# Kernel tuning notes

Hardware: AMD Instinct MI355X
Metric: run time of the kernel (lower is better)

## Reference

```python
import jax, jax.numpy as jnp
import numpy as np

HEADS = 24
HEAD_DIM = 128
DIM = HEADS * HEAD_DIM  # 3072
EPS = 1e-6


def setup_inputs() -> dict:
    key = jax.random.key(0)
    ks = jax.random.split(key, 10)
    B, S_IMG, S_TXT = 1, 2048, 256
    hidden_states = jax.random.normal(ks[0], (B, S_IMG, DIM), jnp.float32)
    encoder_hidden_states = jax.random.normal(ks[1], (B, S_TXT, DIM), jnp.float32)
    # RoPE tables for image tokens, interleaved pair layout [S_IMG, HEAD_DIM]
    inv = 1.0 / (10000.0 ** (np.arange(0, HEAD_DIM, 2, dtype=np.float32) / HEAD_DIM))
    ang = np.arange(S_IMG, dtype=np.float32)[:, None] * inv[None, :]  # [S, Dh/2]
    ang = np.repeat(ang, 2, axis=-1)  # [S, Dh], pairs (2i, 2i+1) share angle
    rope_cos = jnp.asarray(np.cos(ang), jnp.float32)
    rope_sin = jnp.asarray(np.sin(ang), jnp.float32)
    s = 0.02
    wq = jax.random.normal(ks[2], (DIM, DIM), jnp.float32) * s
    wk = jax.random.normal(ks[3], (DIM, DIM), jnp.float32) * s
    wv = jax.random.normal(ks[4], (DIM, DIM), jnp.float32) * s
    wo = jax.random.normal(ks[5], (DIM, DIM), jnp.float32) * s
    bq = jax.random.normal(ks[6], (DIM,), jnp.float32) * s
    bk = jax.random.normal(ks[7], (DIM,), jnp.float32) * s
    bv = jax.random.normal(ks[8], (DIM,), jnp.float32) * s
    bo = jax.random.normal(ks[9], (DIM,), jnp.float32) * s
    norm_q_w = jnp.ones((HEAD_DIM,), jnp.float32)
    norm_k_w = jnp.ones((HEAD_DIM,), jnp.float32)
    return dict(hidden_states=hidden_states, encoder_hidden_states=encoder_hidden_states,
                rope_cos=rope_cos, rope_sin=rope_sin,
                wq=wq, bq=bq, wk=wk, bk=bk, wv=wv, bv=bv,
                norm_q_w=norm_q_w, norm_k_w=norm_k_w, wo=wo, bo=bo)


def _rmsnorm(x, w):
    var = jnp.mean(jnp.square(x), axis=-1, keepdims=True)
    return x * jax.lax.rsqrt(var + EPS) * w


def _rope(x, cos, sin):
    # x [B,H,S,Dh]; diffusers apply_rotary_emb with use_real_unbind_dim=-1:
    # pairs are interleaved (x[2i], x[2i+1]) -> rotated = stack(-imag, real)
    xr = x[..., 0::2]
    xi = x[..., 1::2]
    x_rot = jnp.stack([-xi, xr], axis=-1).reshape(x.shape)
    return x * cos + x_rot * sin


def reference(hidden_states, encoder_hidden_states, rope_cos, rope_sin,
              wq, bq, wk, bk, wv, bv, norm_q_w, norm_k_w, wo, bo):
    B, s_img, D = hidden_states.shape
    s_txt = encoder_hidden_states.shape[1]
    S = s_img + s_txt
    x = jnp.concatenate([hidden_states, encoder_hidden_states], axis=1)  # [B,S,D]

    def proj(w, b):
        return (x @ w + b).reshape(B, S, HEADS, HEAD_DIM).transpose(0, 2, 1, 3)  # [B,H,S,Dh]

    q = _rmsnorm(proj(wq, bq), norm_q_w)
    k = _rmsnorm(proj(wk, bk), norm_k_w)
    v = proj(wv, bv)
    # RoPE on image tokens only
    q = jnp.concatenate([_rope(q[:, :, :s_img], rope_cos, rope_sin), q[:, :, s_img:]], axis=2)
    k = jnp.concatenate([_rope(k[:, :, :s_img], rope_cos, rope_sin), k[:, :, s_img:]], axis=2)
    scale = 1.0 / jnp.sqrt(jnp.float32(HEAD_DIM))
    scores = jnp.einsum('bhqd,bhkd->bhqk', q, k) * scale
    attn = jax.nn.softmax(scores, axis=-1)
    out = jnp.einsum('bhqk,bhkd->bhqd', attn, v)
    out = out.transpose(0, 2, 1, 3).reshape(B, S, D)
    img = out[:, :s_img] @ wo + bo  # to_out[0]; to_out[1] is Dropout(p=0) -> identity
    txt = out[:, s_img:]            # to_add_out is None in this branch
    return img, txt
```

## Files before the change

### kernel.cpp

```cpp
#include <hip/hip_runtime.h>
#include <cstdint>

typedef __bf16 bf16_t;
typedef bf16_t bf16x8 __attribute__((ext_vector_type(8)));
typedef bf16_t bf16x4 __attribute__((ext_vector_type(4)));
typedef float  floatx4 __attribute__((ext_vector_type(4)));

#define S_ALL 2304
#define SIMG  2048
#define NH    24
#define HD    128
#define DIM   3072
#define NQKV  9216

#define SHIFT2 17.312340490667562f
#define QSCALE 0.12751744f

typedef __attribute__((address_space(1))) void* gp1_t;
typedef __attribute__((address_space(3))) void* lp3_t;

__device__ __forceinline__ void async16(const void* g, void* l) {
    __builtin_amdgcn_global_load_lds((gp1_t)(g), (lp3_t)(l), 16, 0, 0);
}
__device__ __forceinline__ floatx4 mfma_bf16(bf16x8 a, bf16x8 b, floatx4 c) {
    return __builtin_amdgcn_mfma_f32_16x16x32_bf16(a, b, c, 0, 0, 0);
}

__global__ __launch_bounds__(256) void k_convert_x(const float* __restrict__ hid,
                                                   const float* __restrict__ enc,
                                                   bf16_t* __restrict__ xb) {
    long i = ((long)blockIdx.x * 256 + threadIdx.x) * 4;
    const long HN = (long)SIMG * DIM;
    float4 f = (i < HN) ? *(const float4*)(hid + i) : *(const float4*)(enc + (i - HN));
    bf16x4 o;
    o[0] = (bf16_t)f.x; o[1] = (bf16_t)f.y; o[2] = (bf16_t)f.z; o[3] = (bf16_t)f.w;
    *(bf16x4*)(xb + i) = o;
}

__global__ __launch_bounds__(256) void k_wT4(const float* __restrict__ wq, const float* __restrict__ wk,
                                             const float* __restrict__ wv, const float* __restrict__ wo,
                                             bf16_t* __restrict__ wTq, bf16_t* __restrict__ woT) {
    __shared__ __align__(16) bf16_t T[64][72];
    int z = blockIdx.z;
    const float* W = (z == 0) ? wq : (z == 1) ? wk : (z == 2) ? wv : wo;
    bf16_t* Wt = (z < 3) ? (wTq + (long)z * DIM * DIM) : woT;
    int r0 = blockIdx.x * 64, c0 = blockIdx.y * 64;
    int tid = threadIdx.x;
    int lr = tid >> 2, lc = (tid & 3) * 16;
    const float* src = W + (long)(r0 + lr) * DIM + c0 + lc;
#pragma unroll
    for (int i = 0; i < 16; i += 4) {
        float4 f = *(const float4*)(src + i);
        T[lr][lc + i + 0] = (bf16_t)f.x;
        T[lr][lc + i + 1] = (bf16_t)f.y;
        T[lr][lc + i + 2] = (bf16_t)f.z;
        T[lr][lc + i + 3] = (bf16_t)f.w;
    }
    __syncthreads();
    bf16x8 a, b;
#pragma unroll
    for (int i = 0; i < 8; i++) a[i] = T[lc + i][lr];
#pragma unroll
    for (int i = 0; i < 8; i++) b[i] = T[lc + 8 + i][lr];
    bf16_t* dst = Wt + (long)(c0 + lr) * DIM + r0 + lc;
    *(bf16x8*)dst = a;
    *(bf16x8*)(dst + 8) = b;
}

__global__ __launch_bounds__(256) void k_gemm_qkv(const bf16_t* __restrict__ A,
                                                  const bf16_t* __restrict__ Bt,
                                                  const float* __restrict__ bq_,
                                                  const float* __restrict__ bk_,
                                                  const float* __restrict__ bv_,
                                                  const float* __restrict__ rope_cos,
                                                  const float* __restrict__ rope_sin,
                                                  const float* __restrict__ nqw,
                                                  const float* __restrict__ nkw,
                                                  bf16_t* __restrict__ qo,
                                                  bf16_t* __restrict__ ko,
                                                  bf16_t* __restrict__ vT) {
    __shared__ __align__(16) char smem[33 * 1024];
    bf16_t* As = (bf16_t*)smem;
    bf16_t* Bs = (bf16_t*)(smem + 16384);
    float* ssq = (float*)(smem + 32768);
    int tid = threadIdx.x;
    int wave = tid >> 6, lane = tid & 63;
    int quad = lane >> 4, l16 = lane & 15;
    long m0 = (long)blockIdx.y * 128, n0 = (long)blockIdx.x * 128;
    int t = blockIdx.x / 24, h = blockIdx.x % 24;
    int wm = (wave >> 1) * 64, wn = (wave & 1) * 64;

    floatx4 zero = {0.f, 0.f, 0.f, 0.f};
    floatx4 acc[4][4];
#pragma unroll
    for (int i = 0; i < 4; i++)
#pragma unroll
        for (int j = 0; j < 4; j++) acc[i][j] = zero;

    int kxor = ((lane & 7) ^ ((lane >> 3) & 7)) * 8;
    const bf16_t* Ag = A + (m0 + wave * 32 + (lane >> 3)) * DIM + kxor;
    const bf16_t* Bg = Bt + (n0 + wave * 32 + (lane >> 3)) * DIM + kxor;
    char* AsB = (char*)As + wave * 4096;
    char* BsB = (char*)Bs + wave * 4096;

    for (int k0 = 0; k0 < DIM; k0 += 64) {
#pragma unroll
        for (int c2 = 0; c2 < 4; ++c2) {
            async16(Ag + (long)c2 * 8 * DIM + k0, AsB + c2 * 1024);
            async16(Bg + (long)c2 * 8 * DIM + k0, BsB + c2 * 1024);
        }
        __syncthreads();
#pragma unroll
        for (int ks = 0; ks < 2; ++ks) {
            bf16x8 af[4], bfr[4];
            int ch = ((ks * 4 + quad) ^ (l16 & 7)) * 8;
#pragma unroll
            for (int i = 0; i < 4; i++)
                af[i] = *(const bf16x8*)&As[(wm + i * 16 + l16) * 64 + ch];
#pragma unroll
            for (int i = 0; i < 4; i++)
                bfr[i] = *(const bf16x8*)&Bs[(wn + i * 16 + l16) * 64 + ch];
#pragma unroll
            for (int i = 0; i < 4; i++)
#pragma unroll
                for (int j = 0; j < 4; j++) acc[i][j] = mfma_bf16(af[i], bfr[j], acc[i][j]);
        }
        __syncthreads();
    }

    int dcol[4];
#pragma unroll
    for (int j = 0; j < 4; j++) dcol[j] = wn + j * 16 + l16;

    if (t == 2) {
        float bias4[4];
#pragma unroll
        for (int j = 0; j < 4; j++) bias4[j] = bv_[h * HD + dcol[j]];
        char* vbuf = smem;
#pragma unroll
        for (int i = 0; i < 4; i++)
#pragma unroll
            for (int r = 0; r < 4; r++) {
                int s_l = wm + i * 16 + quad * 4 + r;
#pragma unroll
                for (int j = 0; j < 4; j++) {
                    int d = dcol[j];
                    int chunk = d * 16 + ((s_l >> 3) ^ (d & 15));
                    *(bf16_t*)(vbuf + chunk * 16 + (s_l & 7) * 2) = (bf16_t)(acc[i][j][r] + bias4[j]);
                }
            }
        __syncthreads();
        int d = tid >> 1, sh = tid & 1;
        bf16_t* dstv = vT + (long)h * HD * S_ALL + (long)d * S_ALL + m0 + sh * 64;
#pragma unroll
        for (int k8 = 0; k8 < 8; ++k8) {
            int s8 = sh * 8 + k8;
            bf16x8 frag = *(const bf16x8*)(vbuf + (d * 16 + (s8 ^ (d & 15))) * 16);
            *(bf16x8*)(dstv + k8 * 8) = frag;
        }
    } else {
        const float* bp = t ? bk_ : bq_;
        const float* nw = t ? nkw : nqw;
        float bias4[4], wv4[4];
#pragma unroll
        for (int j = 0; j < 4; j++) {
            bias4[j] = bp[h * HD + dcol[j]];
            wv4[j] = nw[dcol[j]];
        }
        int wmh = wm >> 6, wnh = wn >> 6;
#pragma unroll
        for (int i = 0; i < 4; i++)
#pragma unroll
            for (int r = 0; r < 4; r++) {
                float s2 = 0.f;
#pragma unroll
                for (int j = 0; j < 4; j++) {
                    float v = acc[i][j][r] + bias4[j];
                    acc[i][j][r] = v;
                    s2 += v * v;
                }
                s2 += __shfl_xor(s2, 1);
                s2 += __shfl_xor(s2, 2);
                s2 += __shfl_xor(s2, 4);
                s2 += __shfl_xor(s2, 8);
                if (l16 == 0) ssq[(wmh * 64 + i * 16 + quad * 4 + r) * 2 + wnh] = s2;
            }
        __syncthreads();
        bf16_t* dst = (t ? ko : qo) + (long)h * S_ALL * HD;
        bool do_rope = (m0 < SIMG);
#pragma unroll
        for (int i = 0; i < 4; i++)
#pragma unroll
            for (int r = 0; r < 4; r++) {
                int row = i * 16 + quad * 4 + r;
                int s_abs = (int)m0 + wm + row;
                float tot = ssq[(wmh * 64 + row) * 2] + ssq[(wmh * 64 + row) * 2 + 1];
                float rms = rsqrtf(tot * (1.0f / 128.0f) + 1e-6f);
                float y[4];
#pragma unroll
                for (int j = 0; j < 4; j++) y[j] = acc[i][j][r] * rms * wv4[j];
                if (do_rope) {
                    const float* cp = rope_cos + (long)s_abs * HD;
                    const float* sp = rope_sin + (long)s_abs * HD;
#pragma unroll
                    for (int j = 0; j < 4; j++) {
                        float c = cp[dcol[j]], sn = sp[dcol[j]];
                        float px = __shfl_xor(y[j], 1);
                        y[j] = y[j] * c + ((l16 & 1) ? px : -px) * sn;
                    }
                }
#pragma unroll
                for (int j = 0; j < 4; j++) {
                    float v = t ? y[j] : y[j] * QSCALE;
                    dst[(long)s_abs * HD + dcol[j]] = (bf16_t)v;
                }
            }
    }
}

__global__ __launch_bounds__(256) void k_gemm_bt(const bf16_t* __restrict__ A,
                                                 const bf16_t* __restrict__ Bt,
                                                 const float* __restrict__ bias,
                                                 bf16_t* __restrict__ Cb, float* __restrict__ Cf,
                                                 int M, int N, int K) {
    __shared__ __align__(16) bf16_t As[128 * 64];
    __shared__ __align__(16) bf16_t Bs[128 * 64];
    int tid = threadIdx.x;
    int wave = tid >> 6, lane = tid & 63;
    int quad = lane >> 4, l16 = lane & 15;
    long m0 = (long)blockIdx.y * 128, n0 = (long)blockIdx.x * 128;
    int wm = (wave >> 1) * 64, wn = (wave & 1) * 64;

    floatx4 zero = {0.f, 0.f, 0.f, 0.f};
    floatx4 acc[4][4];
#pragma unroll
    for (int i = 0; i < 4; i++)
#pragma unroll
        for (int j = 0; j < 4; j++) acc[i][j] = zero;

    int kxor = ((lane & 7) ^ ((lane >> 3) & 7)) * 8;
    const bf16_t* Ag = A + (m0 + wave * 32 + (lane >> 3)) * K + kxor;
    const bf16_t* Bg = Bt + (n0 + wave * 32 + (lane >> 3)) * K + kxor;
    char* AsB = (char*)As + wave * 4096;
    char* BsB = (char*)Bs + wave * 4096;

    for (int k0 = 0; k0 < K; k0 += 64) {
#pragma unroll
        for (int c2 = 0; c2 < 4; ++c2) {
            async16(Ag + (long)c2 * 8 * K + k0, AsB + c2 * 1024);
            async16(Bg + (long)c2 * 8 * K + k0, BsB + c2 * 1024);
        }
        __syncthreads();
#pragma unroll
        for (int ks = 0; ks < 2; ++ks) {
            bf16x8 af[4], bfr[4];
            int ch = ((ks * 4 + quad) ^ (l16 & 7)) * 8;
#pragma unroll
            for (int i = 0; i < 4; i++)
                af[i] = *(const bf16x8*)&As[(wm + i * 16 + l16) * 64 + ch];
#pragma unroll
            for (int i = 0; i < 4; i++)
                bfr[i] = *(const bf16x8*)&Bs[(wn + i * 16 + l16) * 64 + ch];
#pragma unroll
            for (int i = 0; i < 4; i++)
#pragma unroll
                for (int j = 0; j < 4; j++) acc[i][j] = mfma_bf16(af[i], bfr[j], acc[i][j]);
        }
        __syncthreads();
    }

#pragma unroll
    for (int i = 0; i < 4; i++) {
        long rowb = m0 + wm + i * 16 + quad * 4;
#pragma unroll
        for (int j = 0; j < 4; j++) {
            long col = n0 + wn + j * 16 + l16;
            float bv = bias ? bias[col] : 0.0f;
#pragma unroll
            for (int r = 0; r < 4; r++) {
                float v = acc[i][j][r] + bv;
                long idx = (rowb + r) * N + col;
                if (Cb) Cb[idx] = (bf16_t)v;
                else    Cf[idx] = v;
            }
        }
    }
}

__global__ __launch_bounds__(256, 2) void k_attn(const bf16_t* __restrict__ q,
                                                 const bf16_t* __restrict__ k,
                                                 const bf16_t* __restrict__ vT,
                                                 bf16_t* __restrict__ ao,
                                                 float* __restrict__ out_txt) {
    __shared__ __align__(16) bf16_t Ks[64 * 128];
    __shared__ __align__(16) bf16_t VTs[128 * 64];
    __shared__ __align__(16) bf16_t Ps[4][2][16 * 64];
    int tid = threadIdx.x, wave = tid >> 6, lane = tid & 63;
    int quad = lane >> 4, l16 = lane & 15;
    int h = blockIdx.y;
    int q0 = blockIdx.x * 128 + wave * 32;
    const long hbase = (long)h * S_ALL * HD;
    const char* kgb = (const char*)(k + hbase);
    const char* vgb = (const char*)(vT + hbase);

    int koffB[4], voffB[4], slotB[4];
#pragma unroll
    for (int c2 = 0; c2 < 4; ++c2) {
        int L = (wave * 4 + c2) * 64 + lane;
        slotB[c2] = L;
        int rk = L >> 4, ck = (L & 15) ^ (rk & 15);
        koffB[c2] = rk * 256 + ck * 16;
        int rv = L >> 3, cv = (L & 7) ^ (rv & 7) ^ (((rv >> 3) & 1) << 2);
        voffB[c2] = rv * (S_ALL * 2) + cv * 16;
    }

    bf16x8 qf[2][4];
#pragma unroll
    for (int st = 0; st < 2; ++st) {
        const bf16_t* qp = q + hbase + (long)(q0 + st * 16 + l16) * HD + quad * 8;
#pragma unroll
        for (int ks = 0; ks < 4; ++ks) qf[st][ks] = *(const bf16x8*)(qp + ks * 32);
    }

    floatx4 zero = {0.f, 0.f, 0.f, 0.f};
    floatx4 o0[8], o1[8];
#pragma unroll
    for (int ni = 0; ni < 8; ++ni) { o0[ni] = zero; o1[ni] = zero; }
    floatx4 lac0 = zero, lac1 = zero;

    for (int kb = 0; kb < S_ALL / 64; ++kb) {
        const char* kg = kgb + (long)kb * 16384;
        const char* vg = vgb + kb * 128;
#pragma unroll
        for (int c2 = 0; c2 < 4; ++c2) {
            async16(kg + koffB[c2], (char*)Ks + slotB[c2] * 16);
            async16(vg + voffB[c2], (char*)VTs + slotB[c2] * 16);
        }
        __syncthreads();

        floatx4 s0[4], s1[4];
#pragma unroll
        for (int ni = 0; ni < 4; ++ni) { s0[ni] = zero; s1[ni] = zero; }
#pragma unroll
        for (int ks = 0; ks < 4; ++ks)
#pragma unroll
            for (int ni = 0; ni < 4; ++ni) {
                int slot = (ni * 16 + l16) * 16 + ((ks * 4 + quad) ^ l16);
                bf16x8 kf = *(const bf16x8*)&Ks[slot * 8];
                s0[ni] = mfma_bf16(qf[0][ks], kf, s0[ni]);
                s1[ni] = mfma_bf16(qf[1][ks], kf, s1[ni]);
            }

#pragma unroll
        for (int st = 0; st < 2; ++st) {
#pragma unroll
            for (int ni = 0; ni < 4; ++ni) {
                floatx4 sv = st ? s1[ni] : s0[ni];
                floatx4 p;
#pragma unroll
                for (int j = 0; j < 4; ++j) p[j] = __builtin_amdgcn_exp2f(sv[j] - SHIFT2);
                if (st) lac1 += p; else lac0 += p;
#pragma unroll
                for (int j = 0; j < 4; ++j) {
                    int r = quad * 4 + j;
                    int chunk = ((ni * 16 + l16) >> 3) ^ ((r >> 1) & 7);
                    Ps[wave][st][r * 64 + chunk * 8 + (l16 & 7)] = (bf16_t)p[j];
                }
            }
        }

        bf16x8 pf[2][2];
#pragma unroll
        for (int st = 0; st < 2; ++st)
#pragma unroll
            for (int k2 = 0; k2 < 2; ++k2) {
                int chunk = (k2 * 4 + quad) ^ ((l16 >> 1) & 7);
                pf[st][k2] = *(const bf16x8*)&Ps[wave][st][l16 * 64 + chunk * 8];
            }

#pragma unroll
        for (int k2 = 0; k2 < 2; ++k2)
#pragma unroll
            for (int ni = 0; ni < 8; ++ni) {
                int r = ni * 16 + l16;
                int c = (k2 * 4 + quad) ^ (l16 & 7) ^ (((l16 >> 3) & 1) << 2);
                bf16x8 vf = *(const bf16x8*)&VTs[r * 64 + c * 8];
                o0[ni] = mfma_bf16(pf[0][k2], vf, o0[ni]);
                o1[ni] = mfma_bf16(pf[1][k2], vf, o1[ni]);
            }
        __syncthreads();
    }

#pragma unroll
    for (int off = 1; off < 16; off <<= 1) {
#pragma unroll
        for (int j = 0; j < 4; ++j) {
            lac0[j] += __shfl_xor(lac0[j], off);
            lac1[j] += __shfl_xor(lac1[j], off);
        }
    }

#pragma unroll
    for (int st = 0; st < 2; ++st) {
#pragma unroll
        for (int j = 0; j < 4; ++j) {
            float rl = 1.0f / (st ? lac1[j] : lac0[j]);
            int s_row = q0 + st * 16 + quad * 4 + j;
#pragma unroll
            for (int ni = 0; ni < 8; ++ni) {
                float v = (st ? o1[ni][j] : o0[ni][j]) * rl;
                int col = h * HD + ni * 16 + l16;
                ao[(long)s_row * DIM + col] = (bf16_t)v;
                if (s_row >= SIMG) out_txt[(long)(s_row - SIMG) * DIM + col] = v;
            }
        }
    }
}

extern "C" void kernel_launch(void* const* d_in, const int* in_sizes, int n_in,
                              void* d_out, int out_size, void* d_ws, size_t ws_size,
                              hipStream_t stream) {
    const float* hid = (const float*)d_in[0];
    const float* enc = (const float*)d_in[1];
    const float* rope_cos = (const float*)d_in[2];
    const float* rope_sin = (const float*)d_in[3];
    const float* wq = (const float*)d_in[4];
    const float* bq = (const float*)d_in[5];
    const float* wk = (const float*)d_in[6];
    const float* bk = (const float*)d_in[7];
    const float* wv = (const float*)d_in[8];
    const float* bv = (const float*)d_in[9];
    const float* nqw = (const float*)d_in[10];
    const float* nkw = (const float*)d_in[11];
    const float* wo = (const float*)d_in[12];
    const float* bo = (const float*)d_in[13];
    float* out = (float*)d_out;

    char* ws = (char*)d_ws;
    bf16_t* xb   = (bf16_t*)(ws);
    bf16_t* wTq  = (bf16_t*)(ws + 14155776L);
    bf16_t* woT  = (bf16_t*)(ws + 70778880L);
    bf16_t* qb   = (bf16_t*)(ws + 89653248L);
    bf16_t* kbuf = (bf16_t*)(ws + 103809024L);
    bf16_t* vT   = (bf16_t*)(ws + 117964800L);
    bf16_t* ao   = (bf16_t*)(ws + 132120576L);

    k_convert_x<<<6912, 256, 0, stream>>>(hid, enc, xb);
    k_wT4<<<dim3(48, 48, 4), 256, 0, stream>>>(wq, wk, wv, wo, wTq, woT);
    k_gemm_qkv<<<dim3(72, 18), 256, 0, stream>>>(xb, wTq, bq, bk, bv, rope_cos, rope_sin,
                                                 nqw, nkw, qb, kbuf, vT);
    k_attn<<<dim3(18, 24), 256, 0, stream>>>(qb, kbuf, vT, ao, out + (long)SIMG * DIM);
    k_gemm_bt<<<dim3(24, 16), 256, 0, stream>>>(ao, woT, bo, (bf16_t*)nullptr, out, SIMG, DIM, DIM);
}
```

Baseline: 564.5 us.

## Use triple-buffered 256x128 pipelined GEMM with 512-thread blocks for projections

Replaces the synchronous load-then-compute GEMM loop in the QKV and output projection kernels with a shared three-stage LDS pipeline. Async global-to-LDS loads for tile k+2 are issued while MFMAs run on tile k, with raw barriers, explicit vmcnt waits and s_setprio around the MFMA bursts. Block tiles grow to 256x128 with 8 waves, which raises reuse of each B tile. The QKV epilogue is adapted so the V transpose is done in two halves and RMSnorm partial sums cover 256 rows. The cost is a 144KB LDS footprint, which limits each CU to one block, and fewer blocks across the grid, which may cause wave-quantization tails.

```diff
diff --git a/kernel.cpp b/kernel.cpp
--- a/kernel.cpp
+++ b/kernel.cpp
@@ -24,6 +24,9 @@
 }
 __device__ __forceinline__ floatx4 mfma_bf16(bf16x8 a, bf16x8 b, floatx4 c) {
     return __builtin_amdgcn_mfma_f32_16x16x32_bf16(a, b, c, 0, 0, 0);
+}
+__device__ __forceinline__ void barrier_raw() {
+    asm volatile("s_barrier" ::: "memory");
 }
 
 __global__ __launch_bounds__(256) void k_convert_x(const float* __restrict__ hid,
@@ -67,26 +70,109 @@
     *(bf16x8*)(dst + 8) = b;
 }
 
-__global__ __launch_bounds__(256) void k_gemm_qkv(const bf16_t* __restrict__ A,
+__device__ __forceinline__ void gemm_pipe_256x128(const bf16_t* __restrict__ A,
                                                   const bf16_t* __restrict__ Bt,
-                                                  const float* __restrict__ bq_,
-                                                  const float* __restrict__ bk_,
-                                                  const float* __restrict__ bv_,
-                                                  const float* __restrict__ rope_cos,
-                                                  const float* __restrict__ rope_sin,
-                                                  const float* __restrict__ nqw,
-                                                  const float* __restrict__ nkw,
-                                                  bf16_t* __restrict__ qo,
-                                                  bf16_t* __restrict__ ko,
-                                                  bf16_t* __restrict__ vT) {
-    __shared__ __align__(16) char smem[33 * 1024];
-    bf16_t* As = (bf16_t*)smem;
-    bf16_t* Bs = (bf16_t*)(smem + 16384);
-    float* ssq = (float*)(smem + 32768);
+                                                  long m0, long n0, const int K,
+                                                  char* smem, int tid,
+                                                  floatx4 acc[4][4]) {
+    const int wave = tid >> 6, lane = tid & 63;
+    const int quad = lane >> 4, l16 = lane & 15;
+    const int wm = (wave >> 1) * 64;
+    const int wn = (wave & 1) * 64;
+    const int kxor = ((lane & 7) ^ ((lane >> 3) & 7)) * 8;
+    const bf16_t* Ag = A + (m0 + wave * 32 + (lane >> 3)) * K + kxor;
+    const bf16_t* Bg = Bt + (n0 + wave * 16 + (lane >> 3)) * K + kxor;
+    char* Asl = smem + wave * 4096;
+    char* Bsl = smem + 98304 + wave * 2048;
+
+    const int NT = K >> 6;
+
+#pragma unroll
+    for (int c2 = 0; c2 < 4; ++c2) async16(Ag + (long)c2 * 8 * K,      Asl + c2 * 1024);
+#pragma unroll
+    for (int c2 = 0; c2 < 2; ++c2) async16(Bg + (long)c2 * 8 * K,      Bsl + c2 * 1024);
+#pragma unroll
+    for (int c2 = 0; c2 < 4; ++c2) async16(Ag + (long)c2 * 8 * K + 64, Asl + 32768 + c2 * 1024);
+#pragma unroll
+    for (int c2 = 0; c2 < 2; ++c2) async16(Bg + (long)c2 * 8 * K + 64, Bsl + 16384 + c2 * 1024);
+    asm volatile("s_waitcnt vmcnt(6)" ::: "memory");
+    barrier_raw();
+
+    int cur = 0;
+    for (int kt = 0; kt < NT; ++kt) {
+        const bf16_t* As = (const bf16_t*)(smem + cur * 32768);
+        const bf16_t* Bs = (const bf16_t*)(smem + 98304 + cur * 16384);
+        int nxt = cur + 2; if (nxt >= 3) nxt -= 3;
+        char* Asd = Asl + nxt * 32768;
+        char* Bsd = Bsl + nxt * 16384;
+        const long kg = (long)(kt + 2) * 64;
+        const bool issue = (kt < NT - 2);
+
+        bf16x8 af[4], bfr[4];
+        {
+            int ch = (quad ^ (l16 & 7)) * 8;
+#pragma unroll
+            for (int i = 0; i < 4; i++) af[i]  = *(const bf16x8*)&As[(wm + i * 16 + l16) * 64 + ch];
+#pragma unroll
+            for (int j = 0; j < 4; j++) bfr[j] = *(const bf16x8*)&Bs[(wn + j * 16 + l16) * 64 + ch];
+        }
+        if (issue) {
+            async16(Ag + kg,          Asd);
+            async16(Ag + 8 * K + kg,  Asd + 1024);
+            async16(Bg + kg,          Bsd);
+        }
+        barrier_raw();
+        __builtin_amdgcn_s_setprio(1);
+#pragma unroll
+        for (int i = 0; i < 4; i++)
+#pragma unroll
+            for (int j = 0; j < 4; j++) acc[i][j] = mfma_bf16(af[i], bfr[j], acc[i][j]);
+        __builtin_amdgcn_s_setprio(0);
+
+        {
+            int ch = ((4 + quad) ^ (l16 & 7)) * 8;
+#pragma unroll
+            for (int i = 0; i < 4; i++) af[i]  = *(const bf16x8*)&As[(wm + i * 16 + l16) * 64 + ch];
+#pragma unroll
+            for (int j = 0; j < 4; j++) bfr[j] = *(const bf16x8*)&Bs[(wn + j * 16 + l16) * 64 + ch];
+        }
+        if (issue) {
+            async16(Ag + 16 * K + kg, Asd + 2048);
+            async16(Ag + 24 * K + kg, Asd + 3072);
+            async16(Bg + 8 * K + kg,  Bsd + 1024);
+        }
+        barrier_raw();
+        __builtin_amdgcn_s_setprio(1);
+#pragma unroll
+        for (int i = 0; i < 4; i++)
+#pragma unroll
+            for (int j = 0; j < 4; j++) acc[i][j] = mfma_bf16(af[i], bfr[j], acc[i][j]);
+        __builtin_amdgcn_s_setprio(0);
+
+        if (issue) asm volatile("s_waitcnt vmcnt(6)" ::: "memory");
+        else       asm volatile("s_waitcnt vmcnt(0)" ::: "memory");
+        barrier_raw();
+        cur += 1; if (cur >= 3) cur -= 3;
+    }
+}
+
+__global__ __launch_bounds__(512, 2) void k_gemm_qkv(const bf16_t* __restrict__ A,
+                                                     const bf16_t* __restrict__ Bt,
+                                                     const float* __restrict__ bq_,
+                                                     const float* __restrict__ bk_,
+                                                     const float* __restrict__ bv_,
+                                                     const float* __restrict__ rope_cos,
+                                                     const float* __restrict__ rope_sin,
+                                                     const float* __restrict__ nqw,
+                                                     const float* __restrict__ nkw,
+                                                     bf16_t* __restrict__ qo,
+                                                     bf16_t* __restrict__ ko,
+                                                     bf16_t* __restrict__ vT) {
+    __shared__ __align__(16) char smem[147456];
     int tid = threadIdx.x;
     int wave = tid >> 6, lane = tid & 63;
     int quad = lane >> 4, l16 = lane & 15;
-    long m0 = (long)blockIdx.y * 128, n0 = (long)blockIdx.x * 128;
+    long m0 = (long)blockIdx.y * 256, n0 = (long)blockIdx.x * 128;
     int t = blockIdx.x / 24, h = blockIdx.x % 24;
     int wm = (wave >> 1) * 64, wn = (wave & 1) * 64;
 
@@ -97,36 +183,7 @@
 #pragma unroll
         for (int j = 0; j < 4; j++) acc[i][j] = zero;
 
-    int kxor = ((lane & 7) ^ ((lane >> 3) & 7)) * 8;
-    const bf16_t* Ag = A + (m0 + wave * 32 + (lane >> 3)) * DIM + kxor;
-    const bf16_t* Bg = Bt + (n0 + wave * 32 + (lane >> 3)) * DIM + kxor;
-    char* AsB = (char*)As + wave * 4096;
-    char* BsB = (char*)Bs + wave * 4096;
-
-    for (int k0 = 0; k0 < DIM; k0 += 64) {
-#pragma unroll
-        for (int c2 = 0; c2 < 4; ++c2) {
-            async16(Ag + (long)c2 * 8 * DIM + k0, AsB + c2 * 1024);
-            async16(Bg + (long)c2 * 8 * DIM + k0, BsB + c2 * 1024);
-        }
-        __syncthreads();
-#pragma unroll
-        for (int ks = 0; ks < 2; ++ks) {
-            bf16x8 af[4], bfr[4];
-            int ch = ((ks * 4 + quad) ^ (l16 & 7)) * 8;
-#pragma unroll
-            for (int i = 0; i < 4; i++)
-                af[i] = *(const bf16x8*)&As[(wm + i * 16 + l16) * 64 + ch];
-#pragma unroll
-            for (int i = 0; i < 4; i++)
-                bfr[i] = *(const bf16x8*)&Bs[(wn + i * 16 + l16) * 64 + ch];
-#pragma unroll
-            for (int i = 0; i < 4; i++)
-#pragma unroll
-                for (int j = 0; j < 4; j++) acc[i][j] = mfma_bf16(af[i], bfr[j], acc[i][j]);
-        }
-        __syncthreads();
-    }
+    gemm_pipe_256x128(A, Bt, m0, n0, DIM, smem, tid, acc);
 
     int dcol[4];
 #pragma unroll
@@ -137,28 +194,36 @@
 #pragma unroll
         for (int j = 0; j < 4; j++) bias4[j] = bv_[h * HD + dcol[j]];
         char* vbuf = smem;
-#pragma unroll
-        for (int i = 0; i < 4; i++)
-#pragma unroll
-            for (int r = 0; r < 4; r++) {
-                int s_l = wm + i * 16 + quad * 4 + r;
-#pragma unroll
-                for (int j = 0; j < 4; j++) {
-                    int d = dcol[j];
-                    int chunk = d * 16 + ((s_l >> 3) ^ (d & 15));
-                    *(bf16_t*)(vbuf + chunk * 16 + (s_l & 7) * 2) = (bf16_t)(acc[i][j][r] + bias4[j]);
-                }
-            }
-        __syncthreads();
-        int d = tid >> 1, sh = tid & 1;
-        bf16_t* dstv = vT + (long)h * HD * S_ALL + (long)d * S_ALL + m0 + sh * 64;
-#pragma unroll
-        for (int k8 = 0; k8 < 8; ++k8) {
-            int s8 = sh * 8 + k8;
-            bf16x8 frag = *(const bf16x8*)(vbuf + (d * 16 + (s8 ^ (d & 15))) * 16);
-            *(bf16x8*)(dstv + k8 * 8) = frag;
+        int wmi = wave >> 1;
+#pragma unroll
+        for (int half = 0; half < 2; ++half) {
+            if ((wmi >> 1) == half) {
+#pragma unroll
+                for (int i = 0; i < 4; i++)
+#pragma unroll
+                    for (int r = 0; r < 4; r++) {
+                        int s_l = wm - half * 128 + i * 16 + quad * 4 + r;
+#pragma unroll
+                        for (int j = 0; j < 4; j++) {
+                            int d = dcol[j];
+                            int chunk = d * 16 + ((s_l >> 3) ^ (d & 15));
+                            *(bf16_t*)(vbuf + chunk * 16 + (s_l & 7) * 2) = (bf16_t)(acc[i][j][r] + bias4[j]);
+                        }
+                    }
+            }
+            __syncthreads();
+            int d = tid >> 2, sh = tid & 3;
+            bf16_t* dstv = vT + (long)h * HD * S_ALL + (long)d * S_ALL + m0 + half * 128 + sh * 32;
+#pragma unroll
+            for (int k8 = 0; k8 < 4; ++k8) {
+                int s8 = sh * 4 + k8;
+                bf16x8 frag = *(const bf16x8*)(vbuf + (d * 16 + (s8 ^ (d & 15))) * 16);
+                *(bf16x8*)(dstv + k8 * 8) = frag;
+            }
+            __syncthreads();
         }
     } else {
+        float* ssq = (float*)smem;
         const float* bp = t ? bk_ : bq_;
         const float* nw = t ? nkw : nqw;
         float bias4[4], wv4[4];
@@ -167,11 +232,12 @@
             bias4[j] = bp[h * HD + dcol[j]];
             wv4[j] = nw[dcol[j]];
         }
-        int wmh = wm >> 6, wnh = wn >> 6;
+        int wnh = wave & 1;
 #pragma unroll
         for (int i = 0; i < 4; i++)
 #pragma unroll
             for (int r = 0; r < 4; r++) {
+                int row = wm + i * 16 + quad * 4 + r;
                 float s2 = 0.f;
 #pragma unroll
                 for (int j = 0; j < 4; j++) {
@@ -183,7 +249,7 @@
                 s2 += __shfl_xor(s2, 2);
                 s2 += __shfl_xor(s2, 4);
                 s2 += __shfl_xor(s2, 8);
-                if (l16 == 0) ssq[(wmh * 64 + i * 16 + quad * 4 + r) * 2 + wnh] = s2;
+                if (l16 == 0) ssq[row * 2 + wnh] = s2;
             }
         __syncthreads();
         bf16_t* dst = (t ? ko : qo) + (long)h * S_ALL * HD;
@@ -192,9 +258,9 @@
         for (int i = 0; i < 4; i++)
 #pragma unroll
             for (int r = 0; r < 4; r++) {
-                int row = i * 16 + quad * 4 + r;
-                int s_abs = (int)m0 + wm + row;
-                float tot = ssq[(wmh * 64 + row) * 2] + ssq[(wmh * 64 + row) * 2 + 1];
+                int row = wm + i * 16 + quad * 4 + r;
+                int s_abs = (int)m0 + row;
+                float tot = ssq[row * 2] + ssq[row * 2 + 1];
                 float rms = rsqrtf(tot * (1.0f / 128.0f) + 1e-6f);
                 float y[4];
 #pragma unroll
@@ -218,17 +284,16 @@
     }
 }
 
-__global__ __launch_bounds__(256) void k_gemm_bt(const bf16_t* __restrict__ A,
-                                                 const bf16_t* __restrict__ Bt,
-                                                 const float* __restrict__ bias,
-                                                 bf16_t* __restrict__ Cb, float* __restrict__ Cf,
-                                                 int M, int N, int K) {
-    __shared__ __align__(16) bf16_t As[128 * 64];
-    __shared__ __align__(16) bf16_t Bs[128 * 64];
+__global__ __launch_bounds__(512, 2) void k_gemm_bt(const bf16_t* __restrict__ A,
+                                                    const bf16_t* __restrict__ Bt,
+                                                    const float* __restrict__ bias,
+                                                    bf16_t* __restrict__ Cb, float* __restrict__ Cf,
+                                                    int M, int N, int K) {
+    __shared__ __align__(16) char smem[147456];
     int tid = threadIdx.x;
     int wave = tid >> 6, lane = tid & 63;
     int quad = lane >> 4, l16 = lane & 15;
-    long m0 = (long)blockIdx.y * 128, n0 = (long)blockIdx.x * 128;
+    long m0 = (long)blockIdx.y * 256, n0 = (long)blockIdx.x * 128;
     int wm = (wave >> 1) * 64, wn = (wave & 1) * 64;
 
     floatx4 zero = {0.f, 0.f, 0.f, 0.f};
@@ -238,36 +303,7 @@
 #pragma unroll
         for (int j = 0; j < 4; j++) acc[i][j] = zero;
 
-    int kxor = ((lane & 7) ^ ((lane >> 3) & 7)) * 8;
-    const bf16_t* Ag = A + (m0 + wave * 32 + (lane >> 3)) * K + kxor;
-    const bf16_t* Bg = Bt + (n0 + wave * 32 + (lane >> 3)) * K + kxor;
-    char* AsB = (char*)As + wave * 4096;
-    char* BsB = (char*)Bs + wave * 4096;
-
-    for (int k0 = 0; k0 < K; k0 += 64) {
-#pragma unroll
-        for (int c2 = 0; c2 < 4; ++c2) {
-            async16(Ag + (long)c2 * 8 * K + k0, AsB + c2 * 1024);
-            async16(Bg + (long)c2 * 8 * K + k0, BsB + c2 * 1024);
-        }
-        __syncthreads();
-#pragma unroll
-        for (int ks = 0; ks < 2; ++ks) {
-            bf16x8 af[4], bfr[4];
-            int ch = ((ks * 4 + quad) ^ (l16 & 7)) * 8;
-#pragma unroll
-            for (int i = 0; i < 4; i++)
-                af[i] = *(const bf16x8*)&As[(wm + i * 16 + l16) * 64 + ch];
-#pragma unroll
-            for (int i = 0; i < 4; i++)
-                bfr[i] = *(const bf16x8*)&Bs[(wn + i * 16 + l16) * 64 + ch];
-#pragma unroll
-            for (int i = 0; i < 4; i++)
-#pragma unroll
-                for (int j = 0; j < 4; j++) acc[i][j] = mfma_bf16(af[i], bfr[j], acc[i][j]);
-        }
-        __syncthreads();
-    }
+    gemm_pipe_256x128(A, Bt, m0, n0, K, smem, tid, acc);
 
 #pragma unroll
     for (int i = 0; i < 4; i++) {
@@ -447,8 +483,8 @@
 
     k_convert_x<<<6912, 256, 0, stream>>>(hid, enc, xb);
     k_wT4<<<dim3(48, 48, 4), 256, 0, stream>>>(wq, wk, wv, wo, wTq, woT);
-    k_gemm_qkv<<<dim3(72, 18), 256, 0, stream>>>(xb, wTq, bq, bk, bv, rope_cos, rope_sin,
-                                                 nqw, nkw, qb, kbuf, vT);
+    k_gemm_qkv<<<dim3(72, 9), 512, 0, stream>>>(xb, wTq, bq, bk, bv, rope_cos, rope_sin,
+                                                nqw, nkw, qb, kbuf, vT);
     k_attn<<<dim3(18, 24), 256, 0, stream>>>(qb, kbuf, vT, ao, out + (long)SIMG * DIM);
-    k_gemm_bt<<<dim3(24, 16), 256, 0, stream>>>(ao, woT, bo, (bf16_t*)nullptr, out, SIMG, DIM, DIM);
-}
+    k_gemm_bt<<<dim3(24, 8), 512, 0, stream>>>(ao, woT, bo, (bf16_t*)nullptr, out, SIMG, DIM, DIM);
+}
```

Result: faster. 519.4 us (-8.0%).
